# Kernel tuning notes

Measured on AMD Instinct MI355X. Metric: run time of the kernel, lower is better.

Reference implementation:

```python
import jax, jax.numpy as jnp
import numpy as np

N = 32           # signal length (samples)
K_TOTAL = 4      # number of pulses (K=[4], single pulse type)
T = 1.0          # sampling period
RESOLUTION = 64
KNOTS = N * RESOLUTION + 1  # 2049 knots per pulse type
BATCH = 256


def setup_inputs() -> dict:
    key = jax.random.key(0)
    k1, k2 = jax.random.split(key)
    # estimated pulse locations, in [0, 1) (remainder maps everything into [0, N))
    t_k_hat = jax.random.uniform(k1, (BATCH, K_TOTAL), dtype=jnp.float32)
    # c_ReLU: second-difference spline coefficients (uniform init in the module)
    c_relu = jax.random.uniform(k2, (KNOTS,), minval=-0.01, maxval=0.01,
                                dtype=jnp.float32)
    # shift = b_ReLU = -t_phi grid (knot locations), non-trainable in the module
    shift = -(jnp.arange(KNOTS, dtype=jnp.float32) / RESOLUTION)
    # init = phi[0] = 0 for the zero/uniform phi initialisation
    init_val = jnp.zeros((1,), dtype=jnp.float32)
    return {"t_k_hat": t_k_hat, "c_relu": c_relu, "shift": shift,
            "init_val": init_val}


def reference(t_k_hat, c_relu, shift, init_val):
    # fc1 = remainder(t_k/T - n, N), shape [B, K, N] -> [B, N, K]
    n_vec = jnp.arange(N, dtype=t_k_hat.dtype)
    fc1 = jnp.remainder(t_k_hat[..., None] / T - n_vec, N)
    fc1 = jnp.swapaxes(fc1, -1, -2)                      # [B, N, K]
    # train_decoder=True constraint: c[-1] = -sum(c[:-1]) (applied functionally)
    head = c_relu[:-1]
    c_eff = jnp.concatenate([head, -jnp.sum(head, keepdims=True)])
    # Block-diagonal Linear(K_total, knots_tot) with all-ones blocks + shift bias
    # followed by block-diagonal c_ReLU contraction == grouped small matvec:
    # phi_hat[b,n,p] = sum_j relu(fc1[b,n,p] + shift[j]) * c_eff[j] + init
    act = jax.nn.relu(fc1[..., None] + shift)            # [B, N, K, knots]
    phi_hat = jnp.einsum('bnkj,j->bnk', act, c_eff) + init_val
    return phi_hat
```

## Files before the change

kernel.cpp:

```cpp
#include <hip/hip_runtime.h>
#include <hip/hip_bf16.h>

#define NN 32
#define K_TOTAL 4
#define RESOLUTION 64
#define KNOTS (NN * RESOLUTION + 1)
#define BATCH 256
#define HEAD 2048
#define OUT_TOTAL (BATCH * NN * K_TOTAL)

__global__ __launch_bounds__(256) void fused_kernel(const float* __restrict__ t_k,
                                                    const float* __restrict__ c_relu,
                                                    const float* __restrict__ init_val,
                                                    float* __restrict__ out) {
    __shared__ float P1[KNOTS];
    __shared__ float P2[KNOTS];
    __shared__ float tot1[256];
    __shared__ float tot2[256];

    const int t = threadIdx.x;
    const int base = t * 8;

    const float4* __restrict__ c4 = (const float4*)c_relu;
    const float4 ca = c4[2 * t];
    const float4 cb = c4[2 * t + 1];
    float c[8] = {ca.x, ca.y, ca.z, ca.w, cb.x, cb.y, cb.z, cb.w};

    float pre1[8], pre2[8];
    float l1 = 0.0f, l2 = 0.0f;
#pragma unroll
    for (int i = 0; i < 8; ++i) {
        pre1[i] = l1;
        pre2[i] = l2;
        l1 += c[i];
        l2 += (float)(base + i) * c[i];
    }
    tot1[t] = l1;
    tot2[t] = l2;

    for (int off = 1; off < 256; off <<= 1) {
        __syncthreads();
        float a1 = 0.0f, a2 = 0.0f;
        if (t >= off) { a1 = tot1[t - off]; a2 = tot2[t - off]; }
        __syncthreads();
        if (t >= off) { tot1[t] += a1; tot2[t] += a2; }
    }
    __syncthreads();

    const float off1 = (t == 0) ? 0.0f : tot1[t - 1];
    const float off2 = (t == 0) ? 0.0f : tot2[t - 1];
#pragma unroll
    for (int i = 0; i < 8; ++i) {
        P1[base + i] = off1 + pre1[i];
        P2[base + i] = off2 + pre2[i];
    }
    if (t == 255) {
        P1[HEAD] = tot1[255];
        P2[HEAD] = tot2[255];
    }
    __syncthreads();

    const int o = blockIdx.x * 256 + t;
    const int k = o & (K_TOTAL - 1);
    const int n = (o >> 2) & (NN - 1);
    const int b = o >> 7;

    const float tv = t_k[(b << 2) | k];
    float r = tv - (float)n;
    if (r < 0.0f) r += 32.0f;

    const float d = r * 64.0f;
    int m = (int)d;
    if ((float)m < d) ++m;
    if (m > HEAD) m = HEAD;

    out[o] = r * P1[m] - P2[m] * 0.015625f + init_val[0];
}

extern "C" void kernel_launch(void* const* d_in, const int* in_sizes, int n_in,
                              void* d_out, int out_size, void* d_ws, size_t ws_size,
                              hipStream_t stream) {
    const float* t_k_hat  = (const float*)d_in[0];
    const float* c_relu   = (const float*)d_in[1];
    const float* init_val = (const float*)d_in[3];
    float* out = (float*)d_out;

    fused_kernel<<<OUT_TOTAL / 256, 256, 0, stream>>>(t_k_hat, c_relu, init_val, out);
}
```

Baseline: 60.33 us.

## Replace shared-memory block scan with wavefront shuffle scan in double precision

```diff
diff --git a/kernel.cpp b/kernel.cpp
--- a/kernel.cpp
+++ b/kernel.cpp
@@ -15,48 +15,57 @@
                                                     float* __restrict__ out) {
     __shared__ float P1[KNOTS];
     __shared__ float P2[KNOTS];
-    __shared__ float tot1[256];
-    __shared__ float tot2[256];
+    __shared__ double w1[4];
+    __shared__ double w2[4];
 
     const int t = threadIdx.x;
+    const int lane = t & 63;
+    const int wave = t >> 6;
     const int base = t * 8;
 
     const float4* __restrict__ c4 = (const float4*)c_relu;
     const float4 ca = c4[2 * t];
     const float4 cb = c4[2 * t + 1];
-    float c[8] = {ca.x, ca.y, ca.z, ca.w, cb.x, cb.y, cb.z, cb.w};
+    const float c[8] = {ca.x, ca.y, ca.z, ca.w, cb.x, cb.y, cb.z, cb.w};
 
-    float pre1[8], pre2[8];
-    float l1 = 0.0f, l2 = 0.0f;
+    double pre1[8], pre2[8];
+    double l1 = 0.0, l2 = 0.0;
 #pragma unroll
     for (int i = 0; i < 8; ++i) {
         pre1[i] = l1;
         pre2[i] = l2;
-        l1 += c[i];
-        l2 += (float)(base + i) * c[i];
+        l1 += (double)c[i];
+        l2 += (double)(base + i) * (double)c[i];
     }
-    tot1[t] = l1;
-    tot2[t] = l2;
+    const double own1 = l1, own2 = l2;
 
-    for (int off = 1; off < 256; off <<= 1) {
-        __syncthreads();
-        float a1 = 0.0f, a2 = 0.0f;
-        if (t >= off) { a1 = tot1[t - off]; a2 = tot2[t - off]; }
-        __syncthreads();
-        if (t >= off) { tot1[t] += a1; tot2[t] += a2; }
+#pragma unroll
+    for (int d = 1; d < 64; d <<= 1) {
+        const double y1 = __shfl_up(l1, d);
+        const double y2 = __shfl_up(l2, d);
+        if (lane >= d) { l1 += y1; l2 += y2; }
     }
+
+    if (lane == 63) { w1[wave] = l1; w2[wave] = l2; }
     __syncthreads();
 
-    const float off1 = (t == 0) ? 0.0f : tot1[t - 1];
-    const float off2 = (t == 0) ? 0.0f : tot2[t - 1];
+    double woff1 = 0.0, woff2 = 0.0;
+#pragma unroll
+    for (int w = 0; w < 3; ++w) {
+        if (wave > w) { woff1 += w1[w]; woff2 += w2[w]; }
+    }
+
+    const double off1 = woff1 + (l1 - own1);
+    const double off2 = woff2 + (l2 - own2);
+
 #pragma unroll
     for (int i = 0; i < 8; ++i) {
-        P1[base + i] = off1 + pre1[i];
-        P2[base + i] = off2 + pre2[i];
+        P1[base + i] = (float)(off1 + pre1[i]);
+        P2[base + i] = (float)(off2 + pre2[i]);
     }
     if (t == 255) {
-        P1[HEAD] = tot1[255];
-        P2[HEAD] = tot2[255];
+        P1[HEAD] = (float)(woff1 + l1);
+        P2[HEAD] = (float)(woff2 + l2);
     }
     __syncthreads();
 
```

New measurement: 60.05 us. No clear change (-0.5%).
